# Performance work log

Hardware: AMD Instinct MI355X
Metric: run time of the kernel (lower is better)

Reference implementation:

```python
import jax, jax.numpy as jnp
import numpy as np
import math

LMAX = 3  # max output/input angular momentum degree


def _cg(j1, m1, j2, m2, j, m):
    """Clebsch-Gordan coefficient <j1 m1 j2 m2 | j m> (Condon-Shortley)."""
    if m1 + m2 != m or not (abs(j1 - j2) <= j <= j1 + j2):
        return 0.0
    f = math.factorial
    pref = math.sqrt(
        (2 * j + 1)
        * f(j + j1 - j2) * f(j - j1 + j2) * f(j1 + j2 - j) / f(j1 + j2 + j + 1)
        * f(j + m) * f(j - m) * f(j1 - m1) * f(j1 + m1) * f(j2 - m2) * f(j2 + m2)
    )
    kmin = max(0, j2 - j - m1, j1 - j + m2)
    kmax = min(j1 + j2 - j, j1 - m1, j2 + m2)
    s = 0.0
    for k in range(kmin, kmax + 1):
        s += (-1) ** k / (
            f(k) * f(j1 + j2 - j - k) * f(j1 - m1 - k) * f(j2 + m2 - k)
            * f(j - j2 + m1 + k) * f(j - j1 - m2 + k)
        )
    return pref * s


def _cg_mat(l1, l2, l):
    C = np.zeros((2 * l1 + 1, 2 * l2 + 1, 2 * l + 1), dtype=np.float32)
    for m1 in range(-l1, l1 + 1):
        for m2 in range(-l2, l2 + 1):
            m = m1 + m2
            if abs(m) <= l:
                C[m1 + l1, m2 + l2, m + l] = _cg(l1, m1, l2, m2, l, m)
    return C


_CG = {}
for _l1 in range(LMAX + 1):
    for _l2 in range(LMAX + 1):
        for _l in range(abs(_l1 - _l2), min(_l1 + _l2, LMAX) + 1):
            _CG[(_l1, _l2, _l)] = jnp.asarray(_cg_mat(_l1, _l2, _l))


def _cg_product(A, B):
    """Full CG tensor product of two SO3 vec-arrays.

    A[l], B[l]: (2=complex, N, 2l+1, tau). Output degree l collects, for every
    (l1, l2) pair with |l1-l2| <= l <= l1+l2, the channel outer product
    contracted against the CG matrix (cormorant CGProduct semantics).
    """
    parts = [[] for _ in range(LMAX + 1)]
    for l1 in range(LMAX + 1):
        for l2 in range(LMAX + 1):
            Ar, Ai = A[l1][0], A[l1][1]  # (N, 2l1+1, tau1)
            Br, Bi = B[l2][0], B[l2][1]  # (N, 2l2+1, tau2)
            for l in range(abs(l1 - l2), min(l1 + l2, LMAX) + 1):
                C = _CG[(l1, l2, l)]  # (2l1+1, 2l2+1, 2l+1)
                Tr = (jnp.einsum('xyz,nxc,nyd->nzcd', C, Ar, Br)
                      - jnp.einsum('xyz,nxc,nyd->nzcd', C, Ai, Bi))
                Ti = (jnp.einsum('xyz,nxc,nyd->nzcd', C, Ar, Bi)
                      + jnp.einsum('xyz,nxc,nyd->nzcd', C, Ai, Br))
                n = Tr.shape[0]
                T = jnp.stack([Tr, Ti], axis=0).reshape(2, n, 2 * l + 1, -1)
                parts[l].append(T)
    return tuple(jnp.concatenate(p, axis=-1) for p in parts)


def setup_inputs() -> dict:
    key = jax.random.key(0)
    keys = jax.random.split(key, 8)
    N, TAU = 1024, 16
    d = {}
    for l in range(LMAX + 1):
        d[f'A{l}'] = jax.random.normal(keys[l], (2, N, 2 * l + 1, TAU), dtype=jnp.float32)
        d[f'B{l}'] = jax.random.normal(keys[4 + l], (2, N, 2 * l + 1, TAU), dtype=jnp.float32)
    return d


def reference(A0, A1, A2, A3, B0, B1, B2, B3):
    return _cg_product([A0, A1, A2, A3], [B0, B1, B2, B3])
```

## Files before the change

### kernel.cpp

```cpp
#include <hip/hip_runtime.h>


typedef float f32x4 __attribute__((ext_vector_type(4)));

constexpr double dfactc(int n) {
    double r = 1.0;
    for (int i = 2; i <= n; ++i) r *= (double)i;
    return r;
}

constexpr double csqrt(double x) {
    if (x <= 0.0) return 0.0;
    double g = x >= 1.0 ? x : 1.0;
    for (int i = 0; i < 32; ++i) g = 0.5 * (g + x / g);
    return g;
}

constexpr double cg_coef_c(int j1, int m1, int j2, int m2, int j, int m) {
    if (m1 + m2 != m) return 0.0;
    double pref = csqrt((double)(2 * j + 1)
        * dfactc(j + j1 - j2) * dfactc(j - j1 + j2) * dfactc(j1 + j2 - j)
        / dfactc(j1 + j2 + j + 1)
        * dfactc(j + m) * dfactc(j - m) * dfactc(j1 - m1) * dfactc(j1 + m1)
        * dfactc(j2 - m2) * dfactc(j2 + m2));
    int kmin = 0;
    if (j2 - j - m1 > kmin) kmin = j2 - j - m1;
    if (j1 - j + m2 > kmin) kmin = j1 - j + m2;
    int kmax = j1 + j2 - j;
    if (j1 - m1 < kmax) kmax = j1 - m1;
    if (j2 + m2 < kmax) kmax = j2 + m2;
    double s = 0.0;
    for (int k = kmin; k <= kmax; ++k) {
        double d = dfactc(k) * dfactc(j1 + j2 - j - k) * dfactc(j1 - m1 - k)
                 * dfactc(j2 + m2 - k) * dfactc(j - j2 + m1 + k)
                 * dfactc(j - j1 - m2 + k);
        s += (k & 1) ? (-1.0 / d) : (1.0 / d);
    }
    return pref * s;
}

struct PairList {
    int l1[11], l2[11], off[11];
    int np, total;
};

constexpr PairList plist(int L) {
    PairList P{};
    int np = 0, off = 0;
    for (int a = 0; a <= 3; ++a)
    for (int b = 0; b <= 3; ++b) {
        int lo = (a > b) ? (a - b) : (b - a);
        int hi = (a + b < 3) ? (a + b) : 3;
        if (lo <= L && L <= hi) {
            P.l1[np] = a; P.l2[np] = b; P.off[np] = off;
            off += (2 * a + 1) * (2 * b + 1) * (2 * L + 1);
            ++np;
        }
    }
    P.np = np; P.total = off;
    return P;
}

constexpr int cum_floats(int L) {
    int acc = 0;
    for (int l = 0; l < L; ++l) acc += 2 * (2 * l + 1) * 256 * plist(l).np;
    return acc;
}

template <int L> struct CGTabT { float v[plist(L).total]; };

template <int L>
constexpr CGTabT<L> make_cgtab() {
    CGTabT<L> t{};
    constexpr PairList P = plist(L);
    constexpr int zd = 2 * L + 1;
    for (int p = 0; p < P.np; ++p) {
        const int l1 = P.l1[p], l2 = P.l2[p];
        const int yd = 2 * l2 + 1;
        for (int x = 0; x < 2 * l1 + 1; ++x)
            for (int y = 0; y < yd; ++y)
                for (int z = 0; z < zd; ++z)
                    t.v[P.off[p] + (x * yd + y) * zd + z] =
                        (float)cg_coef_c(l1, x - l1, l2, y - l2, L, z - L);
    }
    return t;
}

__constant__ CGTabT<0> CGT0 = make_cgtab<0>();
__constant__ CGTabT<1> CGT1 = make_cgtab<1>();
__constant__ CGTabT<2> CGT2 = make_cgtab<2>();
__constant__ CGTabT<3> CGT3 = make_cgtab<3>();

template <int l1, int l2, int L>
__device__ __forceinline__ void pair_body(
    const float* __restrict__ A0, const float* __restrict__ A1,
    const float* __restrict__ A2, const float* __restrict__ A3,
    const float* __restrict__ B0, const float* __restrict__ B1,
    const float* __restrict__ B2, const float* __restrict__ B3,
    const float* __restrict__ cg, int cgoff,
    unsigned z, unsigned n, unsigned lane,
    float* __restrict__ out, unsigned rowOff, unsigned imagOff, int N)
{
    constexpr int xdim = 2 * l1 + 1, ydim = 2 * l2 + 1, zdim = 2 * L + 1;

    const int s   = (int)z + l1 + l2 - L;
    const int xlo = (s - (ydim - 1) > 0) ? s - (ydim - 1) : 0;
    const int xhi = (s < xdim - 1) ? s : (xdim - 1);

    const unsigned c  = lane >> 2;
    const unsigned d4 = (lane & 3u) << 2;

    const float* Ab = (l1 == 0) ? A0 : (l1 == 1) ? A1 : (l1 == 2) ? A2 : A3;
    const float* Bb = (l2 == 0) ? B0 : (l2 == 1) ? B1 : (l2 == 2) ? B2 : B3;

    const float* Ar = Ab + n * (unsigned)(xdim * 16) + c;
    const float* Ai = Ar + (unsigned)N * (unsigned)(xdim * 16);
    const float* Br = Bb + n * (unsigned)(ydim * 16) + d4;
    const float* Bi = Br + (unsigned)N * (unsigned)(ydim * 16);

    float ar[xdim], ai[xdim];
    #pragma unroll
    for (int x = 0; x < xdim; ++x) { ar[x] = Ar[x * 16]; ai[x] = Ai[x * 16]; }

    const int cgbase = cgoff + s * zdim + (int)z;

    f32x4 accr = {0.f, 0.f, 0.f, 0.f};
    f32x4 acci = {0.f, 0.f, 0.f, 0.f};
    #pragma unroll
    for (int x = 0; x < xdim; ++x) {
        if (x >= xlo && x <= xhi) {
            const float cgv = cg[cgbase + x * (ydim - 1) * zdim];
            const float car = cgv * ar[x];
            const float cai = cgv * ai[x];
            const f32x4 brv = *reinterpret_cast<const f32x4*>(Br + (unsigned)(s - x) * 16u);
            const f32x4 biv = *reinterpret_cast<const f32x4*>(Bi + (unsigned)(s - x) * 16u);
            accr += car * brv - cai * biv;
            acci += car * biv + cai * brv;
        }
    }

    float* oR = out + rowOff + lane * 4u;
    __builtin_nontemporal_store(accr, reinterpret_cast<f32x4*>(oR));
    __builtin_nontemporal_store(acci, reinterpret_cast<f32x4*>(oR + imagOff));
}

template <int L>
__device__ __forceinline__ void doL(unsigned w, unsigned lane,
    const float* __restrict__ A0, const float* __restrict__ A1,
    const float* __restrict__ A2, const float* __restrict__ A3,
    const float* __restrict__ B0, const float* __restrict__ B1,
    const float* __restrict__ B2, const float* __restrict__ B3,
    float* __restrict__ out, int N)
{
    constexpr int NP  = plist(L).np;
    constexpr int ZD  = 2 * L + 1;
    constexpr int CHL = 256 * NP;

    const unsigned p = w % (unsigned)NP;
    const unsigned r = w / (unsigned)NP;
    const unsigned z = r % (unsigned)ZD;
    const unsigned n = r / (unsigned)ZD;

    const unsigned rowOff  = (unsigned)N * (unsigned)cum_floats(L) + w * 256u;
    const unsigned imagOff = (unsigned)N * (unsigned)(ZD * CHL);

    const float* cg = (L == 0) ? CGT0.v : (L == 1) ? CGT1.v
                    : (L == 2) ? CGT2.v : CGT3.v;

#define PB(Lv, K) case K: pair_body<plist(Lv).l1[K], plist(Lv).l2[K], Lv>( \
        A0, A1, A2, A3, B0, B1, B2, B3, cg, plist(Lv).off[K], z, n, lane,  \
        out, rowOff, imagOff, N); break;

    if constexpr (L == 0) {
        switch (p) { PB(0,0) PB(0,1) PB(0,2) PB(0,3) }
    } else if constexpr (L == 1) {
        switch (p) { PB(1,0) PB(1,1) PB(1,2) PB(1,3) PB(1,4) PB(1,5) PB(1,6) PB(1,7) PB(1,8) }
    } else if constexpr (L == 2) {
        switch (p) { PB(2,0) PB(2,1) PB(2,2) PB(2,3) PB(2,4) PB(2,5) PB(2,6) PB(2,7) PB(2,8) PB(2,9) PB(2,10) }
    } else {
        switch (p) { PB(3,0) PB(3,1) PB(3,2) PB(3,3) PB(3,4) PB(3,5) PB(3,6) PB(3,7) PB(3,8) PB(3,9) }
    }
#undef PB
}

__global__ __launch_bounds__(256) void cg_prod_seq(
    const float* __restrict__ A0, const float* __restrict__ A1,
    const float* __restrict__ A2, const float* __restrict__ A3,
    const float* __restrict__ B0, const float* __restrict__ B1,
    const float* __restrict__ B2, const float* __restrict__ B3,
    float* __restrict__ out, int N)
{
    const unsigned gtid = blockIdx.x * 256u + threadIdx.x;
    const unsigned lane = threadIdx.x & 63u;
    unsigned W = gtid >> 6;
    W = (unsigned)__builtin_amdgcn_readfirstlane((int)W);

    const unsigned NN = (unsigned)N;
    if (W < 4u * NN) {
        doL<0>(W,            lane, A0, A1, A2, A3, B0, B1, B2, B3, out, N);
    } else if (W < 31u * NN) {
        doL<1>(W - 4u * NN,  lane, A0, A1, A2, A3, B0, B1, B2, B3, out, N);
    } else if (W < 86u * NN) {
        doL<2>(W - 31u * NN, lane, A0, A1, A2, A3, B0, B1, B2, B3, out, N);
    } else if (W < 156u * NN) {
        doL<3>(W - 86u * NN, lane, A0, A1, A2, A3, B0, B1, B2, B3, out, N);
    }
}

extern "C" void kernel_launch(void* const* d_in, const int* in_sizes, int n_in,
                              void* d_out, int out_size, void* d_ws, size_t ws_size,
                              hipStream_t stream) {
    const float* A0 = (const float*)d_in[0];
    const float* B0 = (const float*)d_in[1];
    const float* A1 = (const float*)d_in[2];
    const float* B1 = (const float*)d_in[3];
    const float* A2 = (const float*)d_in[4];
    const float* B2 = (const float*)d_in[5];
    const float* A3 = (const float*)d_in[6];
    const float* B3 = (const float*)d_in[7];
    float* out = (float*)d_out;
    (void)d_ws; (void)ws_size;

    const int N = in_sizes[0] / 32;

    const int blocks = (156 * N + 3) / 4 / 256 * 256 ? (39 * N) : (39 * N);
    hipLaunchKernelGGL(cg_prod_seq, dim3(39 * N), dim3(256), 0, stream,
                       A0, A1, A2, A3, B0, B1, B2, B3, out, N);
}
```

Before: 338.7 us.

## Assign one block per sample row, looping warps over all output segments

Replaces the flat one-warp-per-segment grid (39*N blocks of 256) with one 512-thread block per sample n. Its 8 warps stride over the 156 (L, z, pair) segments using a constant lookup table and a switch. This is meant to cut launch and scheduling overhead and to improve reuse of the A/B rows for a sample within a workgroup. The cost is a per-iteration constant-table lookup and switch dispatch, and only N=1024 blocks, which gives coarser parallelism and uneven segment counts per warp. A loads also move inside the guarded loop so only the needed ones are issued.

```diff
diff --git a/kernel.cpp b/kernel.cpp
--- a/kernel.cpp
+++ b/kernel.cpp
@@ -91,19 +91,43 @@
 __constant__ CGTabT<2> CGT2 = make_cgtab<2>();
 __constant__ CGTabT<3> CGT3 = make_cgtab<3>();
 
-template <int l1, int l2, int L>
-__device__ __forceinline__ void pair_body(
+struct SegTab { int tid[156]; int z[156]; };
+
+constexpr SegTab make_segtab() {
+    SegTab s{};
+    int i = 0, tidbase = 0;
+    for (int L = 0; L <= 3; ++L) {
+        PairList P = plist(L);
+        int zd = 2 * L + 1;
+        for (int z = 0; z < zd; ++z)
+            for (int p = 0; p < P.np; ++p) {
+                s.tid[i] = tidbase + p;
+                s.z[i]   = z;
+                ++i;
+            }
+        tidbase += P.np;
+    }
+    return s;
+}
+
+__constant__ SegTab SEG = make_segtab();
+
+template <int l1, int l2, int L, int p>
+__device__ __forceinline__ void seg_body(
     const float* __restrict__ A0, const float* __restrict__ A1,
     const float* __restrict__ A2, const float* __restrict__ A3,
     const float* __restrict__ B0, const float* __restrict__ B1,
     const float* __restrict__ B2, const float* __restrict__ B3,
-    const float* __restrict__ cg, int cgoff,
-    unsigned z, unsigned n, unsigned lane,
-    float* __restrict__ out, unsigned rowOff, unsigned imagOff, int N)
+    float* __restrict__ out, int N, unsigned n, unsigned lane, int z)
 {
     constexpr int xdim = 2 * l1 + 1, ydim = 2 * l2 + 1, zdim = 2 * L + 1;
-
-    const int s   = (int)z + l1 + l2 - L;
+    constexpr int CHL  = 256 * plist(L).np;
+    constexpr int CGO  = plist(L).off[p];
+
+    const float* cg = (L == 0) ? CGT0.v : (L == 1) ? CGT1.v
+                    : (L == 2) ? CGT2.v : CGT3.v;
+
+    const int s   = z + l1 + l2 - L;
     const int xlo = (s - (ydim - 1) > 0) ? s - (ydim - 1) : 0;
     const int xhi = (s < xdim - 1) ? s : (xdim - 1);
 
@@ -118,11 +142,7 @@
     const float* Br = Bb + n * (unsigned)(ydim * 16) + d4;
     const float* Bi = Br + (unsigned)N * (unsigned)(ydim * 16);
 
-    float ar[xdim], ai[xdim];
-    #pragma unroll
-    for (int x = 0; x < xdim; ++x) { ar[x] = Ar[x * 16]; ai[x] = Ai[x * 16]; }
-
-    const int cgbase = cgoff + s * zdim + (int)z;
+    const int cgbase = CGO + s * zdim + z;
 
     f32x4 accr = {0.f, 0.f, 0.f, 0.f};
     f32x4 acci = {0.f, 0.f, 0.f, 0.f};
@@ -130,8 +150,8 @@
     for (int x = 0; x < xdim; ++x) {
         if (x >= xlo && x <= xhi) {
             const float cgv = cg[cgbase + x * (ydim - 1) * zdim];
-            const float car = cgv * ar[x];
-            const float cai = cgv * ai[x];
+            const float arv = Ar[x * 16], aiv = Ai[x * 16];
+            const float car = cgv * arv, cai = cgv * aiv;
             const f32x4 brv = *reinterpret_cast<const f32x4*>(Br + (unsigned)(s - x) * 16u);
             const f32x4 biv = *reinterpret_cast<const f32x4*>(Bi + (unsigned)(s - x) * 16u);
             accr += car * brv - cai * biv;
@@ -139,72 +159,46 @@
         }
     }
 
-    float* oR = out + rowOff + lane * 4u;
-    __builtin_nontemporal_store(accr, reinterpret_cast<f32x4*>(oR));
-    __builtin_nontemporal_store(acci, reinterpret_cast<f32x4*>(oR + imagOff));
-}
-
-template <int L>
-__device__ __forceinline__ void doL(unsigned w, unsigned lane,
+    const unsigned base = (unsigned)N * (unsigned)cum_floats(L)
+                        + (n * (unsigned)zdim + (unsigned)z) * (unsigned)CHL
+                        + (unsigned)(p * 256) + lane * 4u;
+    const unsigned imoff = (unsigned)N * (unsigned)(zdim * CHL);
+    __builtin_nontemporal_store(accr, reinterpret_cast<f32x4*>(out + base));
+    __builtin_nontemporal_store(acci, reinterpret_cast<f32x4*>(out + base + imoff));
+}
+
+__global__ __launch_bounds__(512) void cg_prod_rows(
     const float* __restrict__ A0, const float* __restrict__ A1,
     const float* __restrict__ A2, const float* __restrict__ A3,
     const float* __restrict__ B0, const float* __restrict__ B1,
     const float* __restrict__ B2, const float* __restrict__ B3,
     float* __restrict__ out, int N)
 {
-    constexpr int NP  = plist(L).np;
-    constexpr int ZD  = 2 * L + 1;
-    constexpr int CHL = 256 * NP;
-
-    const unsigned p = w % (unsigned)NP;
-    const unsigned r = w / (unsigned)NP;
-    const unsigned z = r % (unsigned)ZD;
-    const unsigned n = r / (unsigned)ZD;
-
-    const unsigned rowOff  = (unsigned)N * (unsigned)cum_floats(L) + w * 256u;
-    const unsigned imagOff = (unsigned)N * (unsigned)(ZD * CHL);
-
-    const float* cg = (L == 0) ? CGT0.v : (L == 1) ? CGT1.v
-                    : (L == 2) ? CGT2.v : CGT3.v;
-
-#define PB(Lv, K) case K: pair_body<plist(Lv).l1[K], plist(Lv).l2[K], Lv>( \
-        A0, A1, A2, A3, B0, B1, B2, B3, cg, plist(Lv).off[K], z, n, lane,  \
-        out, rowOff, imagOff, N); break;
-
-    if constexpr (L == 0) {
-        switch (p) { PB(0,0) PB(0,1) PB(0,2) PB(0,3) }
-    } else if constexpr (L == 1) {
-        switch (p) { PB(1,0) PB(1,1) PB(1,2) PB(1,3) PB(1,4) PB(1,5) PB(1,6) PB(1,7) PB(1,8) }
-    } else if constexpr (L == 2) {
-        switch (p) { PB(2,0) PB(2,1) PB(2,2) PB(2,3) PB(2,4) PB(2,5) PB(2,6) PB(2,7) PB(2,8) PB(2,9) PB(2,10) }
-    } else {
-        switch (p) { PB(3,0) PB(3,1) PB(3,2) PB(3,3) PB(3,4) PB(3,5) PB(3,6) PB(3,7) PB(3,8) PB(3,9) }
+    const unsigned n    = blockIdx.x;
+    const unsigned wid  = threadIdx.x >> 6;
+    const unsigned lane = threadIdx.x & 63u;
+
+#define PB(Lv, BASE, K) case K: \
+    seg_body<plist(Lv).l1[K - BASE], plist(Lv).l2[K - BASE], Lv, K - BASE>( \
+        A0, A1, A2, A3, B0, B1, B2, B3, out, N, n, lane, z); break;
+
+    for (int t = (int)wid; t < 156; t += 8) {
+        const int tid = SEG.tid[t];
+        const int z   = SEG.z[t];
+        switch (tid) {
+            PB(0, 0, 0)   PB(0, 0, 1)   PB(0, 0, 2)   PB(0, 0, 3)
+            PB(1, 4, 4)   PB(1, 4, 5)   PB(1, 4, 6)   PB(1, 4, 7)
+            PB(1, 4, 8)   PB(1, 4, 9)   PB(1, 4, 10)  PB(1, 4, 11)
+            PB(1, 4, 12)
+            PB(2, 13, 13) PB(2, 13, 14) PB(2, 13, 15) PB(2, 13, 16)
+            PB(2, 13, 17) PB(2, 13, 18) PB(2, 13, 19) PB(2, 13, 20)
+            PB(2, 13, 21) PB(2, 13, 22) PB(2, 13, 23)
+            PB(3, 24, 24) PB(3, 24, 25) PB(3, 24, 26) PB(3, 24, 27)
+            PB(3, 24, 28) PB(3, 24, 29) PB(3, 24, 30) PB(3, 24, 31)
+            PB(3, 24, 32) PB(3, 24, 33)
+        }
     }
 #undef PB
-}
-
-__global__ __launch_bounds__(256) void cg_prod_seq(
-    const float* __restrict__ A0, const float* __restrict__ A1,
-    const float* __restrict__ A2, const float* __restrict__ A3,
-    const float* __restrict__ B0, const float* __restrict__ B1,
-    const float* __restrict__ B2, const float* __restrict__ B3,
-    float* __restrict__ out, int N)
-{
-    const unsigned gtid = blockIdx.x * 256u + threadIdx.x;
-    const unsigned lane = threadIdx.x & 63u;
-    unsigned W = gtid >> 6;
-    W = (unsigned)__builtin_amdgcn_readfirstlane((int)W);
-
-    const unsigned NN = (unsigned)N;
-    if (W < 4u * NN) {
-        doL<0>(W,            lane, A0, A1, A2, A3, B0, B1, B2, B3, out, N);
-    } else if (W < 31u * NN) {
-        doL<1>(W - 4u * NN,  lane, A0, A1, A2, A3, B0, B1, B2, B3, out, N);
-    } else if (W < 86u * NN) {
-        doL<2>(W - 31u * NN, lane, A0, A1, A2, A3, B0, B1, B2, B3, out, N);
-    } else if (W < 156u * NN) {
-        doL<3>(W - 86u * NN, lane, A0, A1, A2, A3, B0, B1, B2, B3, out, N);
-    }
 }
 
 extern "C" void kernel_launch(void* const* d_in, const int* in_sizes, int n_in,
@@ -223,7 +217,6 @@
 
     const int N = in_sizes[0] / 32;
 
-    const int blocks = (156 * N + 3) / 4 / 256 * 256 ? (39 * N) : (39 * N);
-    hipLaunchKernelGGL(cg_prod_seq, dim3(39 * N), dim3(256), 0, stream,
+    hipLaunchKernelGGL(cg_prod_rows, dim3(N), dim3(512), 0, stream,
                        A0, A1, A2, A3, B0, B1, B2, B3, out, N);
 }
```

After: 406.0 us. +19.9%, slower.
